# Performance work log

Hardware: AMD Instinct MI355X
Metric: run time of the kernel (lower is better)

Reference implementation:

```python
import jax, jax.numpy as jnp
import numpy as np

NUM_FILTERS = 10


def _peaking(cos_w0, alpha, A):
    aA = alpha * A
    aiA = alpha / A
    Bs = jnp.stack([1 + aA, -2 * cos_w0, 1 - aA], axis=-1)
    As = jnp.stack([1 + aiA, -2 * cos_w0, 1 - aiA], axis=-1)
    return Bs, As


def _low_shelf(cos_w0, alpha, A):
    Ap1, Am1 = A + 1, A - 1
    tsa = 2 * jnp.sqrt(A) * alpha
    Bs = jnp.stack([A * (Ap1 - Am1 * cos_w0 + tsa),
                    2 * A * (Am1 - Ap1 * cos_w0),
                    A * (Ap1 - Am1 * cos_w0 - tsa)], axis=-1)
    As = jnp.stack([Ap1 + Am1 * cos_w0 + tsa,
                    -2 * (Am1 + Ap1 * cos_w0),
                    Ap1 + Am1 * cos_w0 - tsa], axis=-1)
    return Bs, As


def _high_shelf(cos_w0, alpha, A):
    Ap1, Am1 = A + 1, A - 1
    tsa = 2 * jnp.sqrt(A) * alpha
    Bs = jnp.stack([A * (Ap1 + Am1 * cos_w0 + tsa),
                    -2 * A * (Am1 + Ap1 * cos_w0),
                    A * (Ap1 + Am1 * cos_w0 - tsa)], axis=-1)
    As = jnp.stack([Ap1 - Am1 * cos_w0 + tsa,
                    2 * (Am1 - Ap1 * cos_w0),
                    Ap1 - Am1 * cos_w0 - tsa], axis=-1)
    return Bs, As


def _coefficients(w0, q_inv, log_gain):
    # Parameter activations (BaseParametricEqualizerFilter)
    w0 = jnp.pi * jax.nn.sigmoid(w0)
    q_inv = jnp.exp(q_inv)
    A = jnp.exp(log_gain)
    cos_w0 = jnp.cos(w0)
    alpha = jnp.sin(w0) * q_inv * 0.5
    K = w0.shape[-1]
    # split [1, K-2, 1]: low-shelf | peaking | high-shelf
    Bs_ls, As_ls = _low_shelf(cos_w0[..., :1], alpha[..., :1], A[..., :1])
    Bs_pk, As_pk = _peaking(cos_w0[..., 1:K - 1], alpha[..., 1:K - 1], A[..., 1:K - 1])
    Bs_hs, As_hs = _high_shelf(cos_w0[..., K - 1:], alpha[..., K - 1:], A[..., K - 1:])
    Bs = jnp.concatenate([Bs_ls, Bs_pk, Bs_hs], axis=-2)  # (B, C, K, 3)
    As = jnp.concatenate([As_ls, As_pk, As_hs], axis=-2)
    return Bs, As


def _cascade_biquad(x, Bs, As):
    # x: (B, C, L); Bs/As: (B, C, K, 3). Exact cascaded biquad, DF2-transposed.
    b = Bs / As[..., :1]
    a = As / As[..., :1]
    b0, b1, b2 = (jnp.moveaxis(b[..., i], -1, 0) for i in range(3))  # each (K, B, C)
    a1, a2 = (jnp.moveaxis(a[..., i], -1, 0) for i in (1, 2))
    K = b0.shape[0]
    xt = jnp.moveaxis(x, -1, 0)  # (L, B, C)
    s0 = jnp.zeros((K,) + x.shape[:-1], x.dtype)

    def step(carry, x_t):
        s1, s2 = carry  # (K, B, C)
        y = x_t
        ns1, ns2 = [], []
        for k in range(K):  # fixed small cascade, unrolled
            xk = y
            y = b0[k] * xk + s1[k]
            ns1.append(b1[k] * xk - a1[k] * y + s2[k])
            ns2.append(b2[k] * xk - a2[k] * y)
        return (jnp.stack(ns1), jnp.stack(ns2)), y

    _, yt = jax.lax.scan(step, (s0, s0), xt)
    return jnp.moveaxis(yt, 0, -1)  # (B, C, L)


def setup_inputs() -> dict:
    key = jax.random.key(0)
    k1, k2, k3, k4 = jax.random.split(key, 4)
    B, C, L, K = 256, 1, 65536, NUM_FILTERS
    return {
        "input_signals": jax.random.normal(k1, (B, C, L), jnp.float32),
        "w0": jax.random.normal(k2, (B, C, K), jnp.float32),
        "q_inv": jax.random.normal(k3, (B, C, K), jnp.float32),
        "log_gain": jax.random.normal(k4, (B, C, K), jnp.float32) * 0.3,
    }


def reference(input_signals, w0, q_inv, log_gain):
    Bs, As = _coefficients(w0, q_inv, log_gain)
    return _cascade_biquad(input_signals, Bs, As)
```

## Files before the change

kernel.cpp:

```cpp
#include <hip/hip_runtime.h>
#include <math.h>

#ifndef M_PI
#define M_PI 3.14159265358979323846
#endif

#define NFILT   10
#define THREADS 1024
#define CHUNK   64
#define REGS    32
#define LDSS    (CHUNK - REGS)
#define LTOT    (THREADS * CHUNK)
#define NWAVE   (THREADS / 64)

#define WS_STRIDE 576
#define MATS_OFF  96

typedef float v2f __attribute__((ext_vector_type(2)));
__device__ inline v2f mk2(float a, float b) { v2f r; r.x = a; r.y = b; return r; }
#define F2(a,b,c) __builtin_elementwise_fma((a),(b),(c))


__device__ inline void biquad_coefs(int k, double w0r, double qir, double gr,
                                    double* bo, double* ao) {
    const double w0 = M_PI / (1.0 + exp(-w0r));
    const double qi = exp(qir);
    const double A  = exp(gr);
    const double cw = cos(w0);
    const double al = sin(w0) * qi * 0.5;
    double B0, B1, B2, A0, A1, A2;
    if (k == 0) {
        const double Ap1 = A + 1.0, Am1 = A - 1.0, tsa = 2.0 * sqrt(A) * al;
        B0 = A * (Ap1 - Am1 * cw + tsa);
        B1 = 2.0 * A * (Am1 - Ap1 * cw);
        B2 = A * (Ap1 - Am1 * cw - tsa);
        A0 = Ap1 + Am1 * cw + tsa;
        A1 = -2.0 * (Am1 + Ap1 * cw);
        A2 = Ap1 + Am1 * cw - tsa;
    } else if (k == NFILT - 1) {
        const double Ap1 = A + 1.0, Am1 = A - 1.0, tsa = 2.0 * sqrt(A) * al;
        B0 = A * (Ap1 + Am1 * cw + tsa);
        B1 = -2.0 * A * (Am1 + Ap1 * cw);
        B2 = A * (Ap1 + Am1 * cw - tsa);
        A0 = Ap1 - Am1 * cw + tsa;
        A1 = 2.0 * (Am1 - Ap1 * cw);
        A2 = Ap1 - Am1 * cw - tsa;
    } else {
        const double aA = al * A, aiA = al / A;
        B0 = 1.0 + aA;  B1 = -2.0 * cw; B2 = 1.0 - aA;
        A0 = 1.0 + aiA; A1 = B1;        A2 = 1.0 - aiA;
    }
    const double inv = 1.0 / A0;
    bo[0] = B0 * inv; bo[1] = B1 * inv; bo[2] = B2 * inv;
    ao[0] = 1.0;      ao[1] = A1 * inv; ao[2] = A2 * inv;
}

__global__ void eq_precompute_kernel(const float* __restrict__ w0_in,
                                     const float* __restrict__ qinv_in,
                                     const float* __restrict__ gain_in,
                                     float* __restrict__ ws)
{
    const int b = blockIdx.x;
    const int j = threadIdx.x;
    if (j >= NFILT) return;

    double bo[3], ao[3];
    biquad_coefs(j, (double)w0_in[b*NFILT+j], (double)qinv_in[b*NFILT+j],
                 (double)gain_in[b*NFILT+j], bo, ao);

    float* wb = ws + (size_t)b * WS_STRIDE;
    float* cj = wb + j * 8;
    cj[0] = (float)bo[0]; cj[1] = (float)bo[1]; cj[2] = (float)bo[2];
    cj[3] = (float)ao[1]; cj[4] = (float)ao[2];
    cj[5] = (float)(ao[1]*ao[1] - ao[2]);
    cj[6] = (float)(ao[1]*ao[2]);

    double m0 = -ao[1], m1 = -ao[2], m2 = 1.0, m3 = 0.0;
    #pragma unroll
    for (int i = 0; i < 6; ++i) {
        const double n0 = m0*m0 + m1*m2, n1 = m0*m1 + m1*m3;
        const double n2 = m2*m0 + m3*m2, n3 = m2*m1 + m3*m3;
        m0 = n0; m1 = n1; m2 = n2; m3 = n3;
    }
    for (int r = 0; r < 10; ++r) {
        float* mr = wb + MATS_OFF + (j*10 + r)*4;
        mr[0] = (float)m0; mr[1] = (float)m1; mr[2] = (float)m2; mr[3] = (float)m3;
        const double n0 = m0*m0 + m1*m2, n1 = m0*m1 + m1*m3;
        const double n2 = m2*m0 + m3*m2, n3 = m2*m1 + m3*m3;
        m0 = n0; m1 = n1; m2 = n2; m3 = n3;
    }
}


__global__ void
__attribute__((amdgpu_flat_work_group_size(THREADS, THREADS)))
__attribute__((amdgpu_waves_per_eu(4, 4)))
eq_cascade_kernel(const float* __restrict__ x,
                  float* __restrict__ out,
                  const float* __restrict__ ws)
{
    __shared__ float4 sigh[LDSS/4][THREADS];
    __shared__ float2 bnd[THREADS];
    __shared__ float2 waveP[2][NWAVE];

    const int tid  = threadIdx.x;
    const int lane = tid & 63;
    const int wid  = tid >> 6;
    const int b    = blockIdx.x;
    const float* __restrict__ wsb = ws + (size_t)b * WS_STRIDE;

    const float* xb = x   + (size_t)b * LTOT;
    float*       ob = out + (size_t)b * LTOT;

    float sig[REGS];

    const float4* src = reinterpret_cast<const float4*>(xb + (size_t)tid * CHUNK);
    #pragma unroll
    for (int i = 0; i < REGS/4; ++i) {
        const float4 v = src[i];
        sig[4*i+0] = v.x; sig[4*i+1] = v.y; sig[4*i+2] = v.z; sig[4*i+3] = v.w;
    }
    float4 vlast;
    #pragma unroll
    for (int i = 0; i < LDSS/4; ++i) {
        const float4 v = src[REGS/4 + i];
        sigh[i][tid] = v;
        if (i == LDSS/4 - 1) vlast = v;
    }
    bnd[tid] = make_float2(vlast.w, vlast.z);
    __syncthreads();

    float xw1, xw2;
    {
        const float2 t0 = (tid == 0) ? make_float2(0.f, 0.f) : bnd[tid - 1];
        xw1 = t0.x; xw2 = t0.y;
    }
    float i1 = 0.f, i2 = 0.f;
    v2f PA0p = mk2(0.f, 0.f), PA1p = mk2(0.f, 0.f), PA2p = mk2(0.f, 0.f);

    #pragma unroll 1
    for (int j = 0; j < NFILT; ++j) {
        const float* cj = wsb + j*8;
        const float b0 = cj[0], b1c = cj[1], b2 = cj[2];
        const float a1 = cj[3], a2 = cj[4], qa1 = cj[5], qa2 = cj[6];
        const v2f B0v = mk2(b0, b0), B1v = mk2(b1c, b1c), B2v = mk2(b2, b2);
        const v2f A0v = mk2(0.f, -a1), A1v = mk2(-a1, qa1), A2v = mk2(-a2, qa2);
        const float* mb = wsb + MATS_OFF + j*40;

        v2f Zp = mk2(0.f, 0.f);
        v2f Up;
        if (j == 0) {
            Up = mk2(xw2, xw1);
            #pragma unroll
            for (int i = 0; i < REGS/2; ++i) {
                const v2f U  = mk2(sig[2*i], sig[2*i+1]);
                const v2f M1 = mk2(Up.y, U.x);
                const v2f C  = F2(B2v, Up, F2(B1v, M1, B0v*U));
                const v2f Ch = F2(A0v, mk2(C.x, C.x), C);
                const v2f Z  = F2(A2v, mk2(Zp.x, Zp.x), F2(A1v, mk2(Zp.y, Zp.y), Ch));
                sig[2*i] = C.x; sig[2*i+1] = C.y;
                Up = U; Zp = Z;
            }
            #pragma unroll
            for (int i = 0; i < LDSS/4; ++i) {
                const float4 v = sigh[i][tid];
                float4 r;
                #pragma unroll
                for (int h = 0; h < 2; ++h) {
                    const v2f U  = (h == 0) ? mk2(v.x, v.y) : mk2(v.z, v.w);
                    const v2f M1 = mk2(Up.y, U.x);
                    const v2f C  = F2(B2v, Up, F2(B1v, M1, B0v*U));
                    const v2f Ch = F2(A0v, mk2(C.x, C.x), C);
                    const v2f Z  = F2(A2v, mk2(Zp.x, Zp.x), F2(A1v, mk2(Zp.y, Zp.y), Ch));
                    if (h == 0) { r.x = C.x; r.y = C.y; } else { r.z = C.x; r.w = C.y; }
                    Up = U; Zp = Z;
                }
                sigh[i][tid] = r;
            }
        } else {
            Up = mk2(i2, i1);
            #pragma unroll
            for (int i = 0; i < REGS/2; ++i) {
                const v2f S  = mk2(sig[2*i], sig[2*i+1]);
                const v2f Sh = F2(PA0p, mk2(S.x, S.x), S);
                const v2f U  = F2(PA2p, mk2(Up.x, Up.x), F2(PA1p, mk2(Up.y, Up.y), Sh));
                const v2f M1 = mk2(Up.y, U.x);
                const v2f C  = F2(B2v, Up, F2(B1v, M1, B0v*U));
                const v2f Ch = F2(A0v, mk2(C.x, C.x), C);
                const v2f Z  = F2(A2v, mk2(Zp.x, Zp.x), F2(A1v, mk2(Zp.y, Zp.y), Ch));
                sig[2*i] = C.x; sig[2*i+1] = C.y;
                Up = U; Zp = Z;
            }
            #pragma unroll
            for (int i = 0; i < LDSS/4; ++i) {
                const float4 v = sigh[i][tid];
                float4 r;
                #pragma unroll
                for (int h = 0; h < 2; ++h) {
                    const v2f S  = (h == 0) ? mk2(v.x, v.y) : mk2(v.z, v.w);
                    const v2f Sh = F2(PA0p, mk2(S.x, S.x), S);
                    const v2f U  = F2(PA2p, mk2(Up.x, Up.x), F2(PA1p, mk2(Up.y, Up.y), Sh));
                    const v2f M1 = mk2(Up.y, U.x);
                    const v2f C  = F2(B2v, Up, F2(B1v, M1, B0v*U));
                    const v2f Ch = F2(A0v, mk2(C.x, C.x), C);
                    const v2f Z  = F2(A2v, mk2(Zp.x, Zp.x), F2(A1v, mk2(Zp.y, Zp.y), Ch));
                    if (h == 0) { r.x = C.x; r.y = C.y; } else { r.z = C.x; r.w = C.y; }
                    Up = U; Zp = Z;
                }
                sigh[i][tid] = r;
            }
        }

        float Sa = Zp.y, Sb = Zp.x;
        #pragma unroll
        for (int r = 0; r < 6; ++r) {
            const int d = 1 << r;
            const float4 M = *reinterpret_cast<const float4*>(mb + r*4);
            float ta = __shfl_up(Sa, d, 64);
            float tb = __shfl_up(Sb, d, 64);
            const bool act = (lane >= d);
            ta = act ? ta : 0.f;
            tb = act ? tb : 0.f;
            Sa = Sa + M.x * ta + M.y * tb;
            Sb = Sb + M.z * ta + M.w * tb;
        }
        const int buf = j & 1;
        if (lane == 63) waveP[buf][wid] = make_float2(Sa, Sb);
        __syncthreads();

        const float2 Pv = waveP[buf][lane & 15];
        float Tx = Pv.x, Ty = Pv.y;
        #pragma unroll
        for (int l = 0; l < 4; ++l) {
            const int d = 1 << l;
            const float4 M = *reinterpret_cast<const float4*>(mb + (6+l)*4);
            float tx = __shfl_up(Tx, d, 64);
            float ty = __shfl_up(Ty, d, 64);
            const bool act = (lane >= d);
            tx = act ? tx : 0.f;
            ty = act ? ty : 0.f;
            Tx = Tx + M.x * tx + M.y * ty;
            Ty = Ty + M.z * tx + M.w * ty;
        }
        float Vx = __shfl(Tx, wid - 1, 64);
        float Vy = __shfl(Ty, wid - 1, 64);
        if (wid == 0) { Vx = 0.f; Vy = 0.f; }
        #pragma unroll
        for (int r = 0; r < 6; ++r) {
            const float4 M = *reinterpret_cast<const float4*>(mb + r*4);
            const bool bit = (lane >> r) & 1;
            const float nx = M.x * Vx + M.y * Vy;
            const float ny = M.z * Vx + M.w * Vy;
            Vx = bit ? nx : Vx;
            Vy = bit ? ny : Vy;
        }
        {
            float Ea = __shfl_up(Sa, 1, 64);
            float Eb = __shfl_up(Sb, 1, 64);
            const bool l0 = (lane == 0);
            i1 = Vx + (l0 ? 0.f : Ea);
            i2 = Vy + (l0 ? 0.f : Eb);
        }
        PA0p = A0v; PA1p = A1v; PA2p = A2v;
    }

    {
        v2f Up = mk2(i2, i1);
        float4* dst = reinterpret_cast<float4*>(ob + (size_t)tid * CHUNK);
        #pragma unroll
        for (int i = 0; i < REGS/4; ++i) {
            float4 o;
            #pragma unroll
            for (int h = 0; h < 2; ++h) {
                const v2f S  = (h == 0) ? mk2(sig[4*i], sig[4*i+1]) : mk2(sig[4*i+2], sig[4*i+3]);
                const v2f Sh = F2(PA0p, mk2(S.x, S.x), S);
                const v2f U  = F2(PA2p, mk2(Up.x, Up.x), F2(PA1p, mk2(Up.y, Up.y), Sh));
                if (h == 0) { o.x = U.x; o.y = U.y; } else { o.z = U.x; o.w = U.y; }
                Up = U;
            }
            dst[i] = o;
        }
        #pragma unroll
        for (int i = 0; i < LDSS/4; ++i) {
            const float4 v = sigh[i][tid];
            float4 o;
            #pragma unroll
            for (int h = 0; h < 2; ++h) {
                const v2f S  = (h == 0) ? mk2(v.x, v.y) : mk2(v.z, v.w);
                const v2f Sh = F2(PA0p, mk2(S.x, S.x), S);
                const v2f U  = F2(PA2p, mk2(Up.x, Up.x), F2(PA1p, mk2(Up.y, Up.y), Sh));
                if (h == 0) { o.x = U.x; o.y = U.y; } else { o.z = U.x; o.w = U.y; }
                Up = U;
            }
            dst[REGS/4 + i] = o;
        }
    }
}

extern "C" void kernel_launch(void* const* d_in, const int* in_sizes, int n_in,
                              void* d_out, int out_size, void* d_ws, size_t ws_size,
                              hipStream_t stream) {
    const float* x    = (const float*)d_in[0];
    const float* w0   = (const float*)d_in[1];
    const float* qinv = (const float*)d_in[2];
    const float* gain = (const float*)d_in[3];
    float* out = (float*)d_out;
    float* ws  = (float*)d_ws;

    const int B = in_sizes[1] / NFILT;
    eq_precompute_kernel<<<B, 64, 0, stream>>>(w0, qinv, gain, ws);
    eq_cascade_kernel<<<B, THREADS, 0, stream>>>(x, out, ws);
}
```

Measured before the change: 79.93 us.

## Process biquads in pairs with 4-state block scan to halve barrier rounds

Groups the ten biquads into five sections of two, carrying a 4-dimensional state through the chunked parallel prefix scan instead of a 2-dimensional one. Each section's chunk pass runs both filters back-to-back, and the inter-chunk carry uses 4x4 transition matrices precomputed in double. This halves the number of sweeps, block barriers and shuffle-scan rounds per block. In exchange each scan round does more shuffles and matrix FMAs, register pressure rises, and the 64-step matrix built from two cascaded filters may lose float accuracy.

```diff
diff --git a/kernel.cpp b/kernel.cpp
--- a/kernel.cpp
+++ b/kernel.cpp
@@ -6,6 +6,7 @@
 #endif
 
 #define NFILT   10
+#define NSEC    5
 #define THREADS 1024
 #define CHUNK   64
 #define REGS    32
@@ -13,13 +14,29 @@
 #define LTOT    (THREADS * CHUNK)
 #define NWAVE   (THREADS / 64)
 
-#define WS_STRIDE 576
-#define MATS_OFF  96
+#define WS_STRIDE 960
+#define MATS_OFF  160
 
 typedef float v2f __attribute__((ext_vector_type(2)));
 __device__ inline v2f mk2(float a, float b) { v2f r; r.x = a; r.y = b; return r; }
 #define F2(a,b,c) __builtin_elementwise_fma((a),(b),(c))
 
+__device__ inline v2f rec2(v2f C, v2f h, v2f m1, v2f m2, v2f pv) {
+    const v2f Ch = F2(h, mk2(C.x, C.x), C);
+    return F2(m2, mk2(pv.x, pv.x), F2(m1, mk2(pv.y, pv.y), Ch));
+}
+__device__ inline v2f fir2(v2f U, v2f pU, v2f f0, v2f f1, v2f f2c) {
+    return F2(f2c, pU, F2(f1, mk2(pU.y, U.x), f0 * U));
+}
+
+
+__device__ inline void mm4d(const double* X, const double* Y, double* Z) {
+    #pragma unroll
+    for (int r = 0; r < 4; ++r)
+        #pragma unroll
+        for (int c = 0; c < 4; ++c)
+            Z[r*4+c] = X[r*4+0]*Y[c] + X[r*4+1]*Y[4+c] + X[r*4+2]*Y[8+c] + X[r*4+3]*Y[12+c];
+}
 
 __device__ inline void biquad_coefs(int k, double w0r, double qir, double gr,
                                     double* bo, double* ao) {
@@ -62,32 +79,55 @@
 {
     const int b = blockIdx.x;
     const int j = threadIdx.x;
-    if (j >= NFILT) return;
-
-    double bo[3], ao[3];
-    biquad_coefs(j, (double)w0_in[b*NFILT+j], (double)qinv_in[b*NFILT+j],
-                 (double)gain_in[b*NFILT+j], bo, ao);
+    if (j >= NSEC) return;
+
+    double bA[3], aA[3], bB[3], aB[3];
+    const int k0 = 2*j, k1 = 2*j + 1;
+    biquad_coefs(k0, (double)w0_in[b*NFILT+k0], (double)qinv_in[b*NFILT+k0],
+                 (double)gain_in[b*NFILT+k0], bA, aA);
+    biquad_coefs(k1, (double)w0_in[b*NFILT+k1], (double)qinv_in[b*NFILT+k1],
+                 (double)gain_in[b*NFILT+k1], bB, aB);
 
     float* wb = ws + (size_t)b * WS_STRIDE;
-    float* cj = wb + j * 8;
-    cj[0] = (float)bo[0]; cj[1] = (float)bo[1]; cj[2] = (float)bo[2];
-    cj[3] = (float)ao[1]; cj[4] = (float)ao[2];
-    cj[5] = (float)(ao[1]*ao[1] - ao[2]);
-    cj[6] = (float)(ao[1]*ao[2]);
-
-    double m0 = -ao[1], m1 = -ao[2], m2 = 1.0, m3 = 0.0;
+    float* cj = wb + j * 32;
+    cj[0]=0.f;               cj[1]=(float)(-aA[1]);
+    cj[2]=(float)(-aA[1]);   cj[3]=(float)(aA[1]*aA[1]-aA[2]);
+    cj[4]=(float)(-aA[2]);   cj[5]=(float)(aA[1]*aA[2]);
+    cj[6]=(float)bB[0];      cj[7]=(float)bB[0];
+    cj[8]=(float)bB[1];      cj[9]=(float)bB[1];
+    cj[10]=(float)bB[2];     cj[11]=(float)bB[2];
+    cj[12]=0.f;              cj[13]=(float)(-aB[1]);
+    cj[14]=(float)(-aB[1]);  cj[15]=(float)(aB[1]*aB[1]-aB[2]);
+    cj[16]=(float)(-aB[2]);  cj[17]=(float)(aB[1]*aB[2]);
+    cj[18]=(float)bA[0];     cj[19]=(float)bA[0];
+    cj[20]=(float)bA[1];     cj[21]=(float)bA[1];
+    cj[22]=(float)bA[2];     cj[23]=(float)bA[2];
+
+    double M[16], T[16];
     #pragma unroll
-    for (int i = 0; i < 6; ++i) {
-        const double n0 = m0*m0 + m1*m2, n1 = m0*m1 + m1*m3;
-        const double n2 = m2*m0 + m3*m2, n3 = m2*m1 + m3*m3;
-        m0 = n0; m1 = n1; m2 = n2; m3 = n3;
+    for (int c = 0; c < 4; ++c) {
+        double vA1 = (c==0)?1.0:0.0, vA2 = (c==1)?1.0:0.0;
+        double vB1 = (c==2)?1.0:0.0, vB2 = (c==3)?1.0:0.0;
+        for (int t = 0; t < CHUNK; ++t) {
+            const double vA = -aA[1]*vA1 - aA[2]*vA2;
+            const double cB = bB[0]*vA + bB[1]*vA1 + bB[2]*vA2;
+            const double vB = cB - aB[1]*vB1 - aB[2]*vB2;
+            vA2=vA1; vA1=vA; vB2=vB1; vB1=vB;
+        }
+        M[0*4+c]=vA1; M[1*4+c]=vA2; M[2*4+c]=vB1; M[3*4+c]=vB2;
     }
     for (int r = 0; r < 10; ++r) {
-        float* mr = wb + MATS_OFF + (j*10 + r)*4;
-        mr[0] = (float)m0; mr[1] = (float)m1; mr[2] = (float)m2; mr[3] = (float)m3;
-        const double n0 = m0*m0 + m1*m2, n1 = m0*m1 + m1*m3;
-        const double n2 = m2*m0 + m3*m2, n3 = m2*m1 + m3*m3;
-        m0 = n0; m1 = n1; m2 = n2; m3 = n3;
+        float* mr = wb + MATS_OFF + (j*10 + r)*16;
+        #pragma unroll
+        for (int c = 0; c < 4; ++c) {
+            mr[2*c+0]   = (float)M[0*4+c];
+            mr[2*c+1]   = (float)M[1*4+c];
+            mr[8+2*c+0] = (float)M[2*4+c];
+            mr[8+2*c+1] = (float)M[3*4+c];
+        }
+        mm4d(M, M, T);
+        #pragma unroll
+        for (int e = 0; e < 16; ++e) M[e] = T[e];
     }
 }
 
@@ -101,7 +141,7 @@
 {
     __shared__ float4 sigh[LDSS/4][THREADS];
     __shared__ float2 bnd[THREADS];
-    __shared__ float2 waveP[2][NWAVE];
+    __shared__ float4 waveP[2][NWAVE];
 
     const int tid  = threadIdx.x;
     const int lane = tid & 63;
@@ -135,31 +175,30 @@
         const float2 t0 = (tid == 0) ? make_float2(0.f, 0.f) : bnd[tid - 1];
         xw1 = t0.x; xw2 = t0.y;
     }
-    float i1 = 0.f, i2 = 0.f;
-    v2f PA0p = mk2(0.f, 0.f), PA1p = mk2(0.f, 0.f), PA2p = mk2(0.f, 0.f);
+    float i1 = 0.f, i2 = 0.f, i3 = 0.f, i4 = 0.f;
 
     #pragma unroll 1
-    for (int j = 0; j < NFILT; ++j) {
-        const float* cj = wsb + j*8;
-        const float b0 = cj[0], b1c = cj[1], b2 = cj[2];
-        const float a1 = cj[3], a2 = cj[4], qa1 = cj[5], qa2 = cj[6];
-        const v2f B0v = mk2(b0, b0), B1v = mk2(b1c, b1c), B2v = mk2(b2, b2);
-        const v2f A0v = mk2(0.f, -a1), A1v = mk2(-a1, qa1), A2v = mk2(-a2, qa2);
-        const float* mb = wsb + MATS_OFF + j*40;
-
-        v2f Zp = mk2(0.f, 0.f);
-        v2f Up;
+    for (int j = 0; j < NSEC; ++j) {
+        const v2f* cc = reinterpret_cast<const v2f*>(wsb + j*32);
+        const v2f c0 = cc[0], c1 = cc[1], c2 = cc[2];
+        const v2f c3 = cc[3], c4 = cc[4], c5 = cc[5];
+        const v2f c6 = cc[6], c7 = cc[7], c8 = cc[8];
+        const v2f c9 = cc[9], c10 = cc[10], c11 = cc[11];
+        const float* mb = wsb + MATS_OFF + j*160;
+
+        v2f pZA = mk2(0.f, 0.f), pZB = mk2(0.f, 0.f);
+
         if (j == 0) {
-            Up = mk2(xw2, xw1);
+            v2f pU = mk2(xw2, xw1);
             #pragma unroll
             for (int i = 0; i < REGS/2; ++i) {
                 const v2f U  = mk2(sig[2*i], sig[2*i+1]);
-                const v2f M1 = mk2(Up.y, U.x);
-                const v2f C  = F2(B2v, Up, F2(B1v, M1, B0v*U));
-                const v2f Ch = F2(A0v, mk2(C.x, C.x), C);
-                const v2f Z  = F2(A2v, mk2(Zp.x, Zp.x), F2(A1v, mk2(Zp.y, Zp.y), Ch));
-                sig[2*i] = C.x; sig[2*i+1] = C.y;
-                Up = U; Zp = Z;
+                const v2f CA = fir2(U, pU, c9, c10, c11);
+                sig[2*i] = CA.x; sig[2*i+1] = CA.y;
+                const v2f ZA  = rec2(CA, c0, c1, c2, pZA);
+                const v2f CZB = fir2(ZA, pZA, c3, c4, c5);
+                const v2f ZB  = rec2(CZB, c6, c7, c8, pZB);
+                pU = U; pZA = ZA; pZB = ZB;
             }
             #pragma unroll
             for (int i = 0; i < LDSS/4; ++i) {
@@ -168,28 +207,33 @@
                 #pragma unroll
                 for (int h = 0; h < 2; ++h) {
                     const v2f U  = (h == 0) ? mk2(v.x, v.y) : mk2(v.z, v.w);
-                    const v2f M1 = mk2(Up.y, U.x);
-                    const v2f C  = F2(B2v, Up, F2(B1v, M1, B0v*U));
-                    const v2f Ch = F2(A0v, mk2(C.x, C.x), C);
-                    const v2f Z  = F2(A2v, mk2(Zp.x, Zp.x), F2(A1v, mk2(Zp.y, Zp.y), Ch));
-                    if (h == 0) { r.x = C.x; r.y = C.y; } else { r.z = C.x; r.w = C.y; }
-                    Up = U; Zp = Z;
+                    const v2f CA = fir2(U, pU, c9, c10, c11);
+                    const v2f ZA  = rec2(CA, c0, c1, c2, pZA);
+                    const v2f CZB = fir2(ZA, pZA, c3, c4, c5);
+                    const v2f ZB  = rec2(CZB, c6, c7, c8, pZB);
+                    if (h == 0) { r.x = CA.x; r.y = CA.y; } else { r.z = CA.x; r.w = CA.y; }
+                    pU = U; pZA = ZA; pZB = ZB;
                 }
                 sigh[i][tid] = r;
             }
         } else {
-            Up = mk2(i2, i1);
+            const v2f* pc = reinterpret_cast<const v2f*>(wsb + (j-1)*32);
+            const v2f p0 = pc[0], p1 = pc[1], p2 = pc[2];
+            const v2f p3 = pc[3], p4 = pc[4], p5 = pc[5];
+            const v2f p6 = pc[6], p7 = pc[7], p8 = pc[8];
+            v2f pVA = mk2(i2, i1), pVB = mk2(i4, i3);
             #pragma unroll
             for (int i = 0; i < REGS/2; ++i) {
-                const v2f S  = mk2(sig[2*i], sig[2*i+1]);
-                const v2f Sh = F2(PA0p, mk2(S.x, S.x), S);
-                const v2f U  = F2(PA2p, mk2(Up.x, Up.x), F2(PA1p, mk2(Up.y, Up.y), Sh));
-                const v2f M1 = mk2(Up.y, U.x);
-                const v2f C  = F2(B2v, Up, F2(B1v, M1, B0v*U));
-                const v2f Ch = F2(A0v, mk2(C.x, C.x), C);
-                const v2f Z  = F2(A2v, mk2(Zp.x, Zp.x), F2(A1v, mk2(Zp.y, Zp.y), Ch));
-                sig[2*i] = C.x; sig[2*i+1] = C.y;
-                Up = U; Zp = Z;
+                const v2f CAp = mk2(sig[2*i], sig[2*i+1]);
+                const v2f VA = rec2(CAp, p0, p1, p2, pVA);
+                const v2f CB = fir2(VA, pVA, p3, p4, p5);
+                const v2f VB = rec2(CB, p6, p7, p8, pVB);
+                const v2f CA = fir2(VB, pVB, c9, c10, c11);
+                sig[2*i] = CA.x; sig[2*i+1] = CA.y;
+                const v2f ZA  = rec2(CA, c0, c1, c2, pZA);
+                const v2f CZB = fir2(ZA, pZA, c3, c4, c5);
+                const v2f ZB  = rec2(CZB, c6, c7, c8, pZB);
+                pVA = VA; pVB = VB; pZA = ZA; pZB = ZB;
             }
             #pragma unroll
             for (int i = 0; i < LDSS/4; ++i) {
@@ -197,86 +241,100 @@
                 float4 r;
                 #pragma unroll
                 for (int h = 0; h < 2; ++h) {
-                    const v2f S  = (h == 0) ? mk2(v.x, v.y) : mk2(v.z, v.w);
-                    const v2f Sh = F2(PA0p, mk2(S.x, S.x), S);
-                    const v2f U  = F2(PA2p, mk2(Up.x, Up.x), F2(PA1p, mk2(Up.y, Up.y), Sh));
-                    const v2f M1 = mk2(Up.y, U.x);
-                    const v2f C  = F2(B2v, Up, F2(B1v, M1, B0v*U));
-                    const v2f Ch = F2(A0v, mk2(C.x, C.x), C);
-                    const v2f Z  = F2(A2v, mk2(Zp.x, Zp.x), F2(A1v, mk2(Zp.y, Zp.y), Ch));
-                    if (h == 0) { r.x = C.x; r.y = C.y; } else { r.z = C.x; r.w = C.y; }
-                    Up = U; Zp = Z;
+                    const v2f CAp = (h == 0) ? mk2(v.x, v.y) : mk2(v.z, v.w);
+                    const v2f VA = rec2(CAp, p0, p1, p2, pVA);
+                    const v2f CB = fir2(VA, pVA, p3, p4, p5);
+                    const v2f VB = rec2(CB, p6, p7, p8, pVB);
+                    const v2f CA = fir2(VB, pVB, c9, c10, c11);
+                    const v2f ZA  = rec2(CA, c0, c1, c2, pZA);
+                    const v2f CZB = fir2(ZA, pZA, c3, c4, c5);
+                    const v2f ZB  = rec2(CZB, c6, c7, c8, pZB);
+                    if (h == 0) { r.x = CA.x; r.y = CA.y; } else { r.z = CA.x; r.w = CA.y; }
+                    pVA = VA; pVB = VB; pZA = ZA; pZB = ZB;
                 }
                 sigh[i][tid] = r;
             }
         }
 
-        float Sa = Zp.y, Sb = Zp.x;
+        v2f S01 = mk2(pZA.y, pZA.x);
+        v2f S23 = mk2(pZB.y, pZB.x);
         #pragma unroll
         for (int r = 0; r < 6; ++r) {
             const int d = 1 << r;
-            const float4 M = *reinterpret_cast<const float4*>(mb + r*4);
-            float ta = __shfl_up(Sa, d, 64);
-            float tb = __shfl_up(Sb, d, 64);
+            const v2f* mp = reinterpret_cast<const v2f*>(mb + r*16);
+            float t0 = __shfl_up(S01.x, d, 64), t1 = __shfl_up(S01.y, d, 64);
+            float t2 = __shfl_up(S23.x, d, 64), t3 = __shfl_up(S23.y, d, 64);
             const bool act = (lane >= d);
-            ta = act ? ta : 0.f;
-            tb = act ? tb : 0.f;
-            Sa = Sa + M.x * ta + M.y * tb;
-            Sb = Sb + M.z * ta + M.w * tb;
+            t0 = act ? t0 : 0.f; t1 = act ? t1 : 0.f;
+            t2 = act ? t2 : 0.f; t3 = act ? t3 : 0.f;
+            S01 = F2(mp[0], mk2(t0,t0), S01); S01 = F2(mp[1], mk2(t1,t1), S01);
+            S01 = F2(mp[2], mk2(t2,t2), S01); S01 = F2(mp[3], mk2(t3,t3), S01);
+            S23 = F2(mp[4], mk2(t0,t0), S23); S23 = F2(mp[5], mk2(t1,t1), S23);
+            S23 = F2(mp[6], mk2(t2,t2), S23); S23 = F2(mp[7], mk2(t3,t3), S23);
         }
         const int buf = j & 1;
-        if (lane == 63) waveP[buf][wid] = make_float2(Sa, Sb);
+        if (lane == 63) waveP[buf][wid] = make_float4(S01.x, S01.y, S23.x, S23.y);
         __syncthreads();
 
-        const float2 Pv = waveP[buf][lane & 15];
-        float Tx = Pv.x, Ty = Pv.y;
+        const float4 Pv = waveP[buf][lane & 15];
+        v2f T01 = mk2(Pv.x, Pv.y), T23 = mk2(Pv.z, Pv.w);
         #pragma unroll
         for (int l = 0; l < 4; ++l) {
             const int d = 1 << l;
-            const float4 M = *reinterpret_cast<const float4*>(mb + (6+l)*4);
-            float tx = __shfl_up(Tx, d, 64);
-            float ty = __shfl_up(Ty, d, 64);
+            const v2f* mp = reinterpret_cast<const v2f*>(mb + (6+l)*16);
+            float t0 = __shfl_up(T01.x, d, 64), t1 = __shfl_up(T01.y, d, 64);
+            float t2 = __shfl_up(T23.x, d, 64), t3 = __shfl_up(T23.y, d, 64);
             const bool act = (lane >= d);
-            tx = act ? tx : 0.f;
-            ty = act ? ty : 0.f;
-            Tx = Tx + M.x * tx + M.y * ty;
-            Ty = Ty + M.z * tx + M.w * ty;
-        }
-        float Vx = __shfl(Tx, wid - 1, 64);
-        float Vy = __shfl(Ty, wid - 1, 64);
-        if (wid == 0) { Vx = 0.f; Vy = 0.f; }
+            t0 = act ? t0 : 0.f; t1 = act ? t1 : 0.f;
+            t2 = act ? t2 : 0.f; t3 = act ? t3 : 0.f;
+            T01 = F2(mp[0], mk2(t0,t0), T01); T01 = F2(mp[1], mk2(t1,t1), T01);
+            T01 = F2(mp[2], mk2(t2,t2), T01); T01 = F2(mp[3], mk2(t3,t3), T01);
+            T23 = F2(mp[4], mk2(t0,t0), T23); T23 = F2(mp[5], mk2(t1,t1), T23);
+            T23 = F2(mp[6], mk2(t2,t2), T23); T23 = F2(mp[7], mk2(t3,t3), T23);
+        }
+        float v0 = __shfl(T01.x, wid - 1, 64), v1 = __shfl(T01.y, wid - 1, 64);
+        float v2 = __shfl(T23.x, wid - 1, 64), v3 = __shfl(T23.y, wid - 1, 64);
+        if (wid == 0) { v0 = v1 = v2 = v3 = 0.f; }
+        v2f V01 = mk2(v0, v1), V23 = mk2(v2, v3);
         #pragma unroll
         for (int r = 0; r < 6; ++r) {
-            const float4 M = *reinterpret_cast<const float4*>(mb + r*4);
+            const v2f* mp = reinterpret_cast<const v2f*>(mb + r*16);
+            v2f N01 = mp[0] * mk2(V01.x, V01.x);
+            N01 = F2(mp[1], mk2(V01.y, V01.y), N01);
+            N01 = F2(mp[2], mk2(V23.x, V23.x), N01);
+            N01 = F2(mp[3], mk2(V23.y, V23.y), N01);
+            v2f N23 = mp[4] * mk2(V01.x, V01.x);
+            N23 = F2(mp[5], mk2(V01.y, V01.y), N23);
+            N23 = F2(mp[6], mk2(V23.x, V23.x), N23);
+            N23 = F2(mp[7], mk2(V23.y, V23.y), N23);
             const bool bit = (lane >> r) & 1;
-            const float nx = M.x * Vx + M.y * Vy;
-            const float ny = M.z * Vx + M.w * Vy;
-            Vx = bit ? nx : Vx;
-            Vy = bit ? ny : Vy;
-        }
-        {
-            float Ea = __shfl_up(Sa, 1, 64);
-            float Eb = __shfl_up(Sb, 1, 64);
-            const bool l0 = (lane == 0);
-            i1 = Vx + (l0 ? 0.f : Ea);
-            i2 = Vy + (l0 ? 0.f : Eb);
-        }
-        PA0p = A0v; PA1p = A1v; PA2p = A2v;
+            V01 = bit ? N01 : V01;
+            V23 = bit ? N23 : V23;
+        }
+        float e0 = __shfl_up(S01.x, 1, 64), e1 = __shfl_up(S01.y, 1, 64);
+        float e2 = __shfl_up(S23.x, 1, 64), e3 = __shfl_up(S23.y, 1, 64);
+        if (lane == 0) { e0 = e1 = e2 = e3 = 0.f; }
+        i1 = V01.x + e0; i2 = V01.y + e1; i3 = V23.x + e2; i4 = V23.y + e3;
     }
 
     {
-        v2f Up = mk2(i2, i1);
+        const v2f* pc = reinterpret_cast<const v2f*>(wsb + (NSEC-1)*32);
+        const v2f p0 = pc[0], p1 = pc[1], p2 = pc[2];
+        const v2f p3 = pc[3], p4 = pc[4], p5 = pc[5];
+        const v2f p6 = pc[6], p7 = pc[7], p8 = pc[8];
+        v2f pVA = mk2(i2, i1), pVB = mk2(i4, i3);
         float4* dst = reinterpret_cast<float4*>(ob + (size_t)tid * CHUNK);
         #pragma unroll
         for (int i = 0; i < REGS/4; ++i) {
             float4 o;
             #pragma unroll
             for (int h = 0; h < 2; ++h) {
-                const v2f S  = (h == 0) ? mk2(sig[4*i], sig[4*i+1]) : mk2(sig[4*i+2], sig[4*i+3]);
-                const v2f Sh = F2(PA0p, mk2(S.x, S.x), S);
-                const v2f U  = F2(PA2p, mk2(Up.x, Up.x), F2(PA1p, mk2(Up.y, Up.y), Sh));
-                if (h == 0) { o.x = U.x; o.y = U.y; } else { o.z = U.x; o.w = U.y; }
-                Up = U;
+                const v2f CAp = (h == 0) ? mk2(sig[4*i], sig[4*i+1]) : mk2(sig[4*i+2], sig[4*i+3]);
+                const v2f VA = rec2(CAp, p0, p1, p2, pVA);
+                const v2f CB = fir2(VA, pVA, p3, p4, p5);
+                const v2f VB = rec2(CB, p6, p7, p8, pVB);
+                if (h == 0) { o.x = VB.x; o.y = VB.y; } else { o.z = VB.x; o.w = VB.y; }
+                pVA = VA; pVB = VB;
             }
             dst[i] = o;
         }
@@ -286,11 +344,12 @@
             float4 o;
             #pragma unroll
             for (int h = 0; h < 2; ++h) {
-                const v2f S  = (h == 0) ? mk2(v.x, v.y) : mk2(v.z, v.w);
-                const v2f Sh = F2(PA0p, mk2(S.x, S.x), S);
-                const v2f U  = F2(PA2p, mk2(Up.x, Up.x), F2(PA1p, mk2(Up.y, Up.y), Sh));
-                if (h == 0) { o.x = U.x; o.y = U.y; } else { o.z = U.x; o.w = U.y; }
-                Up = U;
+                const v2f CAp = (h == 0) ? mk2(v.x, v.y) : mk2(v.z, v.w);
+                const v2f VA = rec2(CAp, p0, p1, p2, pVA);
+                const v2f CB = fir2(VA, pVA, p3, p4, p5);
+                const v2f VB = rec2(CB, p6, p7, p8, pVB);
+                if (h == 0) { o.x = VB.x; o.y = VB.y; } else { o.z = VB.x; o.w = VB.y; }
+                pVA = VA; pVB = VB;
             }
             dst[REGS/4 + i] = o;
         }
```

New measurement: 88.67 us. 1.11x slower.

## Replace block barrier with decoupled wave-to-wave flag chain for cross-wave prefix

Applied to the files above, without the earlier changes.

Replaces the per-filter __syncthreads plus 16-wave Kogge-Stone scan of wave totals with a serial chained look-back. Each wave spins on a volatile LDS flag from its predecessor, folds in that predecessor's inclusive total, and publishes its own. This removes a full block barrier per filter stage and lets waves run ahead on later work. The cost is a serial dependency chain across 16 waves and spin-waiting that can stall under scheduling.

```diff
diff --git a/kernel.cpp b/kernel.cpp
--- a/kernel.cpp
+++ b/kernel.cpp
@@ -101,7 +101,8 @@
 {
     __shared__ float4 sigh[LDSS/4][THREADS];
     __shared__ float2 bnd[THREADS];
-    __shared__ float2 waveP[2][NWAVE];
+    __shared__ float2 waveT[NFILT][NWAVE];
+    volatile __shared__ int wflag[NWAVE];
 
     const int tid  = threadIdx.x;
     const int lane = tid & 63;
@@ -128,6 +129,7 @@
         if (i == LDSS/4 - 1) vlast = v;
     }
     bnd[tid] = make_float2(vlast.w, vlast.z);
+    if (tid < NWAVE) wflag[tid] = 0;
     __syncthreads();
 
     float xw1, xw2;
@@ -224,27 +226,24 @@
             Sa = Sa + M.x * ta + M.y * tb;
             Sb = Sb + M.z * ta + M.w * tb;
         }
-        const int buf = j & 1;
-        if (lane == 63) waveP[buf][wid] = make_float2(Sa, Sb);
-        __syncthreads();
-
-        const float2 Pv = waveP[buf][lane & 15];
-        float Tx = Pv.x, Ty = Pv.y;
-        #pragma unroll
-        for (int l = 0; l < 4; ++l) {
-            const int d = 1 << l;
-            const float4 M = *reinterpret_cast<const float4*>(mb + (6+l)*4);
-            float tx = __shfl_up(Tx, d, 64);
-            float ty = __shfl_up(Ty, d, 64);
-            const bool act = (lane >= d);
-            tx = act ? tx : 0.f;
-            ty = act ? ty : 0.f;
-            Tx = Tx + M.x * tx + M.y * ty;
-            Ty = Ty + M.z * tx + M.w * ty;
-        }
-        float Vx = __shfl(Tx, wid - 1, 64);
-        float Vy = __shfl(Ty, wid - 1, 64);
-        if (wid == 0) { Vx = 0.f; Vy = 0.f; }
+
+        float Tpx = 0.f, Tpy = 0.f;
+        if (wid > 0) {
+            while (wflag[wid - 1] < j + 1) { }
+            __threadfence_block();
+            volatile const float* wtp = (volatile const float*)&waveT[j][wid - 1];
+            Tpx = wtp[0]; Tpy = wtp[1];
+        }
+        if (lane == 63) {
+            const float4 M6 = *reinterpret_cast<const float4*>(mb + 6*4);
+            const float Twx = Sa + M6.x * Tpx + M6.y * Tpy;
+            const float Twy = Sb + M6.z * Tpx + M6.w * Tpy;
+            waveT[j][wid] = make_float2(Twx, Twy);
+            __threadfence_block();
+            wflag[wid] = j + 1;
+        }
+
+        float Vx = Tpx, Vy = Tpy;
         #pragma unroll
         for (int r = 0; r < 6; ++r) {
             const float4 M = *reinterpret_cast<const float4*>(mb + r*4);
```

Result: no change. 79.12 us (-1.0%).
